# Kernel tuning notes

Hardware: AMD Instinct MI355X
Metric: run time of the kernel (lower is better)

Reference implementation:

```python
import jax, jax.numpy as jnp
import numpy as np

N_NODES = 100000
N_EDGES = 1600000
F_IN = 128
F_HID = 128
BN_EPS = 1e-5


def setup_inputs() -> dict:
    key = jax.random.key(0)
    ks = jax.random.split(key, 8)
    x = jax.random.normal(ks[0], (N_NODES, F_IN), dtype=jnp.float32)
    edge_row = jax.random.randint(ks[1], (N_EDGES,), 0, N_NODES, dtype=jnp.int32)
    edge_col = jax.random.randint(ks[2], (N_EDGES,), 0, N_NODES, dtype=jnp.int32)
    edge_weight = jax.random.uniform(ks[3], (N_EDGES,), dtype=jnp.float32)
    # Glorot-ish init for the two GCN layer weights
    W1 = jax.random.normal(ks[4], (F_IN, F_HID), dtype=jnp.float32) * (1.0 / np.sqrt(F_IN))
    b1 = jnp.zeros((F_HID,), dtype=jnp.float32)
    W2 = jax.random.normal(ks[5], (F_HID, F_HID), dtype=jnp.float32) * (1.0 / np.sqrt(F_HID))
    b2 = jnp.zeros((F_HID,), dtype=jnp.float32)
    gamma = jnp.ones((F_HID,), dtype=jnp.float32)
    beta = jnp.zeros((F_HID,), dtype=jnp.float32)
    return {"x": x, "edge_row": edge_row, "edge_col": edge_col,
            "edge_weight": edge_weight, "W1": W1, "b1": b1,
            "W2": W2, "b2": b2, "gamma": gamma, "beta": beta}


def _spmm(row, col, w, dense):
    # sparse [N,N] @ dense [N,F] via gather + segment_sum (COO)
    gathered = dense[col] * w[:, None]           # [E, F]
    return jax.ops.segment_sum(gathered, row, num_segments=N_NODES)


def _batchnorm(h, gamma, beta):
    # BatchNorm1d in training mode: batch statistics over node dim
    mean = jnp.mean(h, axis=0)
    var = jnp.var(h, axis=0)
    return gamma * (h - mean) * jax.lax.rsqrt(var + BN_EPS) + beta


def reference(x, edge_row, edge_col, edge_weight, W1, b1, W2, b2, gamma, beta):
    # Layer 1: GCN conv = adj @ (x @ W1) + b1
    h = _spmm(edge_row, edge_col, edge_weight, x @ W1) + b1
    # BN -> ReLU (dropout is identity in deterministic/eval reference)
    h = jax.nn.relu(_batchnorm(h, gamma, beta))
    # Layer 2: GCN conv
    out = _spmm(edge_row, edge_col, edge_weight, h @ W2) + b2
    return out
```

## Files before the change

kernel.cpp:

```cpp
#include <hip/hip_runtime.h>

#define F    128
#define FQ   32
#define FU   64
#define RPB  128
#define BSH  7
#define TILE 2048
#define SCAP 4096
#define LSTR 68

typedef __attribute__((ext_vector_type(8))) short short8;
typedef __attribute__((ext_vector_type(4))) float f32x4;
typedef __attribute__((ext_vector_type(4))) unsigned int u32x4;

__device__ __forceinline__ unsigned int f2bf2(float a, float b) {
    unsigned int ua = __float_as_uint(a);
    unsigned int ub = __float_as_uint(b);
    ua = (ua + 0x7fffu + ((ua >> 16) & 1u)) >> 16;
    ub = (ub + 0x7fffu + ((ub >> 16) & 1u)) >> 16;
    return ua | (ub << 16);
}
__device__ __forceinline__ unsigned short f2bf1(float a) {
    unsigned int ua = __float_as_uint(a);
    return (unsigned short)((ua + 0x7fffu + ((ua >> 16) & 1u)) >> 16);
}

__global__ __launch_bounds__(256) void wconv_kernel(const float* __restrict__ W1,
                                                    const float* __restrict__ W2,
                                                    unsigned int* __restrict__ Wt1,
                                                    unsigned int* __restrict__ Wt2) {
    const float* W = blockIdx.x ? W2 : W1;
    unsigned int* Wt = blockIdx.x ? Wt2 : Wt1;
    int f = threadIdx.x & 127;
    int kh = (threadIdx.x >> 7) * 64;
    #pragma unroll
    for (int k8 = 0; k8 < 8; ++k8) {
        int k0 = kh + k8 * 8;
        float v[8];
        #pragma unroll
        for (int i = 0; i < 8; ++i) v[i] = W[(size_t)(k0 + i) * F + f];
        uint4 pk;
        pk.x = f2bf2(v[0], v[1]);
        pk.y = f2bf2(v[2], v[3]);
        pk.z = f2bf2(v[4], v[5]);
        pk.w = f2bf2(v[6], v[7]);
        *(uint4*)&Wt[f * 64 + k0 / 2] = pk;
    }
}

template <bool BN>
__global__ __launch_bounds__(256) void gemm_kernel(const void* __restrict__ Xv,
                                                   const unsigned int* __restrict__ Wt,
                                                   const float* __restrict__ stats,
                                                   const float* __restrict__ gamma,
                                                   const float* __restrict__ beta,
                                                   float invN,
                                                   unsigned int* __restrict__ Hb,
                                                   int nNodes) {
    __shared__ unsigned int XtU[64 * LSTR];
    __shared__ unsigned int WtU[128 * LSTR];

    const int tid = threadIdx.x;
    const int bn0 = blockIdx.x * 64;

    {
        int f = tid >> 1;
        int kh = (tid & 1) * 32;
        const uint4* Wg4 = (const uint4*)Wt;
        #pragma unroll
        for (int j = 0; j < 8; ++j) {
            uint4 pk = Wg4[f * 16 + (kh >> 2) + j];
            *(uint4*)&WtU[f * LSTR + kh + j * 4] = pk;
        }
    }
    {
        const int kq = tid & 31;
        float4 a4, c4;
        if (BN) {
            float4 s  = ((const float4*)stats)[kq];
            float4 sq = ((const float4*)(stats + 128))[kq];
            float4 g4 = ((const float4*)gamma)[kq];
            float4 b4 = ((const float4*)beta)[kq];
            float m;
            m = s.x * invN; a4.x = g4.x * rsqrtf(sq.x * invN - m * m + 1e-5f); c4.x = b4.x - m * a4.x;
            m = s.y * invN; a4.y = g4.y * rsqrtf(sq.y * invN - m * m + 1e-5f); c4.y = b4.y - m * a4.y;
            m = s.z * invN; a4.z = g4.z * rsqrtf(sq.z * invN - m * m + 1e-5f); c4.z = b4.z - m * a4.z;
            m = s.w * invN; a4.w = g4.w * rsqrtf(sq.w * invN - m * m + 1e-5f); c4.w = b4.w - m * a4.w;
        }
        #pragma unroll
        for (int it = 0; it < 8; ++it) {
            int i = tid + it * 256;
            int n = i >> 5;
            int node = bn0 + n;
            uint2 pk = make_uint2(0u, 0u);
            if (BN) {
                uint2 raw = make_uint2(0u, 0u);
                if (node < nNodes) raw = ((const uint2*)Xv)[(size_t)node * 32 + kq];
                float4 v;
                v.x = __uint_as_float(raw.x << 16);
                v.y = __uint_as_float(raw.x & 0xffff0000u);
                v.z = __uint_as_float(raw.y << 16);
                v.w = __uint_as_float(raw.y & 0xffff0000u);
                v.x = fmaxf(fmaf(a4.x, v.x, c4.x), 0.f);
                v.y = fmaxf(fmaf(a4.y, v.y, c4.y), 0.f);
                v.z = fmaxf(fmaf(a4.z, v.z, c4.z), 0.f);
                v.w = fmaxf(fmaf(a4.w, v.w, c4.w), 0.f);
                pk = make_uint2(f2bf2(v.x, v.y), f2bf2(v.z, v.w));
            } else {
                float4 v = make_float4(0.f, 0.f, 0.f, 0.f);
                if (node < nNodes) v = ((const float4*)Xv)[(size_t)node * FQ + kq];
                pk = make_uint2(f2bf2(v.x, v.y), f2bf2(v.z, v.w));
            }
            *(uint2*)&XtU[n * LSTR + kq * 2] = pk;
        }
    }
    __syncthreads();

    const int l = tid & 63;
    const int wv = tid >> 6;
    const int quad = l >> 4, lo = l & 15;
    const int fb = wv * 32;

    f32x4 acc[4][2];
    #pragma unroll
    for (int nt = 0; nt < 4; ++nt)
        #pragma unroll
        for (int ft = 0; ft < 2; ++ft) acc[nt][ft] = (f32x4){0.f, 0.f, 0.f, 0.f};

    #pragma unroll
    for (int kc = 0; kc < 4; ++kc) {
        int koff = kc * 16 + quad * 4;
        short8 a[4], b[2];
        #pragma unroll
        for (int nt = 0; nt < 4; ++nt)
            a[nt] = *(const short8*)&XtU[(nt * 16 + lo) * LSTR + koff];
        #pragma unroll
        for (int ft = 0; ft < 2; ++ft)
            b[ft] = *(const short8*)&WtU[(fb + ft * 16 + lo) * LSTR + koff];
        #pragma unroll
        for (int nt = 0; nt < 4; ++nt)
            #pragma unroll
            for (int ft = 0; ft < 2; ++ft)
                acc[nt][ft] = __builtin_amdgcn_mfma_f32_16x16x32_bf16(
                    a[nt], b[ft], acc[nt][ft], 0, 0, 0);
    }

    unsigned short* Hs = (unsigned short*)Hb;
    #pragma unroll
    for (int nt = 0; nt < 4; ++nt) {
        #pragma unroll
        for (int reg = 0; reg < 4; ++reg) {
            int node = bn0 + nt * 16 + quad * 4 + reg;
            if (node < nNodes) {
                #pragma unroll
                for (int ft = 0; ft < 2; ++ft)
                    Hs[(size_t)node * F + fb + ft * 16 + lo] = f2bf1(acc[nt][ft][reg]);
            }
        }
    }
}

__global__ __launch_bounds__(256) void histo_kernel(const int* __restrict__ row,
                                                    int* __restrict__ hist,
                                                    int NB, int E) {
    __shared__ int h[1024];
    int t = threadIdx.x;
    for (int i = t; i < NB; i += 256) h[i] = 0;
    __syncthreads();
    int base = blockIdx.x * TILE + t * 8;
    if (base + 7 < E) {
        int4 a = ((const int4*)row)[(base >> 2) + 0];
        int4 b = ((const int4*)row)[(base >> 2) + 1];
        atomicAdd(&h[a.x >> BSH], 1); atomicAdd(&h[a.y >> BSH], 1);
        atomicAdd(&h[a.z >> BSH], 1); atomicAdd(&h[a.w >> BSH], 1);
        atomicAdd(&h[b.x >> BSH], 1); atomicAdd(&h[b.y >> BSH], 1);
        atomicAdd(&h[b.z >> BSH], 1); atomicAdd(&h[b.w >> BSH], 1);
    } else {
        for (int j = 0; j < 8; ++j)
            if (base + j < E) atomicAdd(&h[row[base + j] >> BSH], 1);
    }
    __syncthreads();
    for (int i = t; i < NB; i += 256) hist[(size_t)blockIdx.x * NB + i] = h[i];
}

__global__ __launch_bounds__(256) void btot_kernel(const int* __restrict__ hist,
                                                   int* __restrict__ total,
                                                   int nT, int NB) {
    int b = blockIdx.x;
    int s = 0;
    for (int t = threadIdx.x; t < nT; t += 256) s += hist[(size_t)t * NB + b];
    __shared__ int red[256];
    red[threadIdx.x] = s;
    __syncthreads();
    for (int o = 128; o > 0; o >>= 1) {
        if (threadIdx.x < o) red[threadIdx.x] += red[threadIdx.x + o];
        __syncthreads();
    }
    if (threadIdx.x == 0) total[b] = red[0];
}

__global__ __launch_bounds__(1024) void bstart_kernel(const int* __restrict__ total,
                                                      int* __restrict__ start,
                                                      int NB, int E) {
    __shared__ int sh[1024];
    int t = threadIdx.x;
    int v = (t < NB) ? total[t] : 0;
    sh[t] = v;
    __syncthreads();
    #pragma unroll
    for (int o = 1; o < 1024; o <<= 1) {
        int add = (t >= o) ? sh[t - o] : 0;
        __syncthreads();
        sh[t] += add;
        __syncthreads();
    }
    if (t < NB) start[t] = sh[t] - v;
    if (t == 0) start[NB] = E;
}

__global__ __launch_bounds__(1024) void boff_kernel(const int* __restrict__ hist,
                                                    const int* __restrict__ start,
                                                    int* __restrict__ off,
                                                    int nT, int NB) {
    __shared__ int sh[1024];
    int b = blockIdx.x, t = threadIdx.x;
    int v = (t < nT) ? hist[(size_t)t * NB + b] : 0;
    sh[t] = v;
    __syncthreads();
    #pragma unroll
    for (int o = 1; o < 1024; o <<= 1) {
        int add = (t >= o) ? sh[t - o] : 0;
        __syncthreads();
        sh[t] += add;
        __syncthreads();
    }
    if (t < nT) off[(size_t)b * nT + t] = start[b] + sh[t] - v;
}

__global__ __launch_bounds__(256) void bplace_kernel(const int* __restrict__ row,
                                                     const int* __restrict__ col,
                                                     const float* __restrict__ w,
                                                     const int* __restrict__ off,
                                                     int2* __restrict__ tmp,
                                                     int nT, int NB, int E) {
    __shared__ int h[1024];
    int t = threadIdx.x, tile = blockIdx.x;
    for (int i = t; i < NB; i += 256) h[i] = 0;
    __syncthreads();
    int base = tile * TILE + t * 8;
    int r[8], c[8];
    float ww[8];
    int nv = 0;
    if (base + 7 < E) {
        int4 ra = ((const int4*)row)[(base >> 2) + 0];
        int4 rb = ((const int4*)row)[(base >> 2) + 1];
        int4 ca = ((const int4*)col)[(base >> 2) + 0];
        int4 cb = ((const int4*)col)[(base >> 2) + 1];
        float4 wa = ((const float4*)w)[(base >> 2) + 0];
        float4 wb = ((const float4*)w)[(base >> 2) + 1];
        r[0] = ra.x; r[1] = ra.y; r[2] = ra.z; r[3] = ra.w;
        r[4] = rb.x; r[5] = rb.y; r[6] = rb.z; r[7] = rb.w;
        c[0] = ca.x; c[1] = ca.y; c[2] = ca.z; c[3] = ca.w;
        c[4] = cb.x; c[5] = cb.y; c[6] = cb.z; c[7] = cb.w;
        ww[0] = wa.x; ww[1] = wa.y; ww[2] = wa.z; ww[3] = wa.w;
        ww[4] = wb.x; ww[5] = wb.y; ww[6] = wb.z; ww[7] = wb.w;
        nv = 8;
    } else {
        for (int j = 0; j < 8; ++j)
            if (base + j < E) { r[nv] = row[base + j]; c[nv] = col[base + j];
                                ww[nv] = w[base + j]; ++nv; }
    }
    #pragma unroll 8
    for (int j = 0; j < 8; ++j) {
        if (j >= nv) break;
        int b = r[j] >> BSH;
        int rank = atomicAdd(&h[b], 1);
        int pos = off[(size_t)b * nT + tile] + rank;
        tmp[pos] = make_int2(((r[j] & (RPB - 1)) << 25) | c[j], __float_as_int(ww[j]));
    }
}

__global__ __launch_bounds__(256) void bsort_kernel(const int2* __restrict__ tmp,
                                                    const int* __restrict__ start,
                                                    int2* __restrict__ pairs,
                                                    int* __restrict__ rowptr,
                                                    int N, int NB, int E) {
    __shared__ int cntB[RPB];
    __shared__ int cntS[RPB];
    __shared__ int sc[RPB];
    __shared__ int2 outP[SCAP];
    int b = blockIdx.x, t = threadIdx.x;
    int s0 = start[b], s1 = start[b + 1];
    int len = s1 - s0;
    if (len > SCAP) len = SCAP;

    if (t < RPB) cntB[t] = 0;
    __syncthreads();

    int2 p[16];
    int np = 0;
    #pragma unroll
    for (int k = 0; k < 16; ++k) {
        int i = t + k * 256;
        if (i < len) { p[k] = tmp[s0 + i]; ++np; }
    }
    #pragma unroll
    for (int k = 0; k < 16; ++k) {
        if (k >= np) break;
        atomicAdd(&cntB[((unsigned)p[k].x) >> 25], 1);
    }
    __syncthreads();
    int val = (t < RPB) ? cntB[t] : 0;
    if (t < RPB) sc[t] = val;
    __syncthreads();
    #pragma unroll
    for (int o = 1; o < RPB; o <<= 1) {
        int add = (t < RPB && t >= o) ? sc[t - o] : 0;
        __syncthreads();
        if (t < RPB) sc[t] += add;
        __syncthreads();
    }
    if (t < RPB) { int ex = sc[t] - val; cntB[t] = ex; cntS[t] = ex; }
    __syncthreads();
    #pragma unroll
    for (int k = 0; k < 16; ++k) {
        if (k >= np) break;
        int rl = ((unsigned)p[k].x) >> 25;
        int lr = atomicAdd(&cntB[rl], 1);
        outP[lr] = make_int2(p[k].x & 0x1ffffff, p[k].y);
    }
    __syncthreads();
    for (int i = t; i < len; i += 256) pairs[s0 + i] = outP[i];
    int r0 = b * RPB;
    if (t < RPB && r0 + t < N) rowptr[r0 + t] = s0 + cntS[t];
    if (b == NB - 1 && t == 0) rowptr[N] = E;
}

template <bool BF16OUT>
__global__ __launch_bounds__(256) void spmm_csr_kernel(const int* __restrict__ rowptr,
                                                       const int2* __restrict__ pairs,
                                                       const unsigned int* __restrict__ Hb,
                                                       const float* __restrict__ bias,
                                                       void* __restrict__ outv, int N) {
    int r = blockIdx.x * 4 + (threadIdx.x >> 6);
    if (r >= N) return;
    const int l = threadIdx.x & 63;
    const int g = l >> 4, q = l & 15;
    const uint4* H4 = (const uint4*)Hb;

    float acc[8];
    #pragma unroll
    for (int j = 0; j < 8; ++j) acc[j] = 0.f;

    int i = rowptr[r], end = rowptr[r + 1];

    for (; i + 16 <= end; i += 16) {
        int2 p[4];
        uint4 gv[4];
        #pragma unroll
        for (int k = 0; k < 4; ++k) p[k] = pairs[i + 4 * k + g];
        #pragma unroll
        for (int k = 0; k < 4; ++k) gv[k] = H4[(size_t)p[k].x * 16 + q];
        #pragma unroll
        for (int k = 0; k < 4; ++k) {
            float wt = __int_as_float(p[k].y);
            unsigned int uu[4] = {gv[k].x, gv[k].y, gv[k].z, gv[k].w};
            #pragma unroll
            for (int j = 0; j < 4; ++j) {
                acc[2 * j]     = fmaf(wt, __uint_as_float(uu[j] << 16), acc[2 * j]);
                acc[2 * j + 1] = fmaf(wt, __uint_as_float(uu[j] & 0xffff0000u), acc[2 * j + 1]);
            }
        }
    }
    for (; i + 4 <= end; i += 4) {
        int2 p = pairs[i + g];
        uint4 gv = H4[(size_t)p.x * 16 + q];
        float wt = __int_as_float(p.y);
        unsigned int uu[4] = {gv.x, gv.y, gv.z, gv.w};
        #pragma unroll
        for (int j = 0; j < 4; ++j) {
            acc[2 * j]     = fmaf(wt, __uint_as_float(uu[j] << 16), acc[2 * j]);
            acc[2 * j + 1] = fmaf(wt, __uint_as_float(uu[j] & 0xffff0000u), acc[2 * j + 1]);
        }
    }
    if (i < end) {
        int e = i + g;
        int2 p = (e < end) ? pairs[e] : make_int2(0, 0);
        uint4 gv = H4[(size_t)p.x * 16 + q];
        float wt = __int_as_float(p.y);
        unsigned int uu[4] = {gv.x, gv.y, gv.z, gv.w};
        #pragma unroll
        for (int j = 0; j < 4; ++j) {
            acc[2 * j]     = fmaf(wt, __uint_as_float(uu[j] << 16), acc[2 * j]);
            acc[2 * j + 1] = fmaf(wt, __uint_as_float(uu[j] & 0xffff0000u), acc[2 * j + 1]);
        }
    }

    #pragma unroll
    for (int j = 0; j < 8; ++j) {
        acc[j] += __shfl_xor(acc[j], 16, 64);
        acc[j] += __shfl_xor(acc[j], 32, 64);
    }

    if (g == 0) {
        if (bias) {
            float4 b0 = ((const float4*)bias)[q * 2];
            float4 b1 = ((const float4*)bias)[q * 2 + 1];
            acc[0] += b0.x; acc[1] += b0.y; acc[2] += b0.z; acc[3] += b0.w;
            acc[4] += b1.x; acc[5] += b1.y; acc[6] += b1.z; acc[7] += b1.w;
        }
        if (BF16OUT) {
            uint4 pk;
            pk.x = f2bf2(acc[0], acc[1]);
            pk.y = f2bf2(acc[2], acc[3]);
            pk.z = f2bf2(acc[4], acc[5]);
            pk.w = f2bf2(acc[6], acc[7]);
            ((uint4*)outv)[(size_t)r * 16 + q] = pk;
        } else {
            f32x4 v0 = (f32x4){acc[0], acc[1], acc[2], acc[3]};
            f32x4 v1 = (f32x4){acc[4], acc[5], acc[6], acc[7]};
            f32x4* O = (f32x4*)outv;
            __builtin_nontemporal_store(v0, &O[(size_t)r * 32 + q * 2]);
            __builtin_nontemporal_store(v1, &O[(size_t)r * 32 + q * 2 + 1]);
        }
    }
}

__global__ __launch_bounds__(256) void bnstats_kernel(const unsigned int* __restrict__ Hu,
                                                      float* __restrict__ sums,
                                                      int nNodes) {
    int u = threadIdx.x & 63;
    int g = threadIdx.x >> 6;
    int stride = gridDim.x * 4;
    float s0 = 0.f, s1 = 0.f, q0 = 0.f, q1 = 0.f;
    for (int n = blockIdx.x * 4 + g; n < nNodes; n += stride) {
        unsigned int v = Hu[(size_t)n * FU + u];
        float a = __uint_as_float(v << 16);
        float b = __uint_as_float(v & 0xffff0000u);
        s0 += a; s1 += b;
        q0 = fmaf(a, a, q0); q1 = fmaf(b, b, q1);
    }
    __shared__ float4 red[256];
    red[threadIdx.x] = make_float4(s0, s1, q0, q1);
    __syncthreads();
    if (g == 0) {
        float4 r0 = red[u], r1 = red[64 + u], r2 = red[128 + u], r3 = red[192 + u];
        atomicAdd(&sums[2 * u],           r0.x + r1.x + r2.x + r3.x);
        atomicAdd(&sums[2 * u + 1],       r0.y + r1.y + r2.y + r3.y);
        atomicAdd(&sums[128 + 2 * u],     r0.z + r1.z + r2.z + r3.z);
        atomicAdd(&sums[128 + 2 * u + 1], r0.w + r1.w + r2.w + r3.w);
    }
}

extern "C" void kernel_launch(void* const* d_in, const int* in_sizes, int n_in,
                              void* d_out, int out_size, void* d_ws, size_t ws_size,
                              hipStream_t stream) {
    const float* x    = (const float*)d_in[0];
    const int*   erow = (const int*)d_in[1];
    const int*   ecol = (const int*)d_in[2];
    const float* ew   = (const float*)d_in[3];
    const float* W1   = (const float*)d_in[4];
    const float* W2   = (const float*)d_in[6];
    const float* b2   = (const float*)d_in[7];
    const float* gmm  = (const float*)d_in[8];
    const float* beta = (const float*)d_in[9];
    float* out = (float*)d_out;

    const int N = in_sizes[0] / F;
    const int E = in_sizes[1];

    const int NB = (N + RPB - 1) / RPB;
    const int nT = (E + TILE - 1) / TILE;

    unsigned int* buf1   = (unsigned int*)d_ws;
    unsigned int* Hb     = buf1 + (size_t)N * FU;
    float*        stats  = (float*)(Hb + (size_t)N * FU);
    unsigned int* wt1    = (unsigned int*)(stats + 256);
    unsigned int* wt2    = wt1 + 8192;
    int*          rowptr = (int*)(wt2 + 8192);
    int*          start  = rowptr + N + 2;
    int*          total  = start + 1028;
    int*          hist   = total + 1024;
    int*          off    = hist + (size_t)nT * NB;
    int2*         tmp    = (int2*)(off + (size_t)NB * nT);
    int2*         pairs  = tmp + E;

    const int gemmGrid = (N + 63) / 64;
    const int spmmGrid = (N + 3) / 4;

    hipMemsetAsync(stats, 0, 256 * sizeof(float), stream);

    wconv_kernel<<<2, 256, 0, stream>>>(W1, W2, wt1, wt2);

    histo_kernel<<<nT, 256, 0, stream>>>(erow, hist, NB, E);
    btot_kernel<<<NB, 256, 0, stream>>>(hist, total, nT, NB);
    bstart_kernel<<<1, 1024, 0, stream>>>(total, start, NB, E);
    boff_kernel<<<NB, 1024, 0, stream>>>(hist, start, off, nT, NB);
    bplace_kernel<<<nT, 256, 0, stream>>>(erow, ecol, ew, off, tmp, nT, NB, E);
    bsort_kernel<<<NB, 256, 0, stream>>>(tmp, start, pairs, rowptr, N, NB, E);

    gemm_kernel<false><<<gemmGrid, 256, 0, stream>>>(x, wt1, nullptr, nullptr,
                                                     nullptr, 0.f, Hb, N);
    spmm_csr_kernel<true><<<spmmGrid, 256, 0, stream>>>(rowptr, pairs, Hb,
                                                        nullptr, buf1, N);
    bnstats_kernel<<<400, 256, 0, stream>>>(buf1, stats, N);
    gemm_kernel<true><<<gemmGrid, 256, 0, stream>>>(buf1, wt2, stats, gmm, beta,
                                                    1.0f / (float)N, Hb, N);
    spmm_csr_kernel<false><<<spmmGrid, 256, 0, stream>>>(rowptr, pairs, Hb,
                                                         b2, out, N);
}
```

Measured before the change: 397.2 us.

## Merge preprocessing launches and co-schedule first GEMM with edge placement

Folds the weight conversion into the histogram kernel, merges the bucket-start scan into the per-bucket offset kernel, and runs the first-layer GEMM blocks in the same launch as the edge bucket placement. Each tile now covers 8192 edges instead of 2048, so there are fewer histogram rows and offset scan entries. The aim is to cut launch count and let the independent GEMM overlap the memory-bound placement pass. In exchange, every offset block recomputes the bucket-total scan, and fewer tiles means less parallelism in the histogram and placement phases.

```diff
diff --git a/kernel.cpp b/kernel.cpp
--- a/kernel.cpp
+++ b/kernel.cpp
@@ -5,13 +5,12 @@
 #define FU   64
 #define RPB  128
 #define BSH  7
-#define TILE 2048
+#define TILE 8192
 #define SCAP 4096
 #define LSTR 68
 
 typedef __attribute__((ext_vector_type(8))) short short8;
 typedef __attribute__((ext_vector_type(4))) float f32x4;
-typedef __attribute__((ext_vector_type(4))) unsigned int u32x4;
 
 __device__ __forceinline__ unsigned int f2bf2(float a, float b) {
     unsigned int ua = __float_as_uint(a);
@@ -25,43 +24,19 @@
     return (unsigned short)((ua + 0x7fffu + ((ua >> 16) & 1u)) >> 16);
 }
 
-__global__ __launch_bounds__(256) void wconv_kernel(const float* __restrict__ W1,
-                                                    const float* __restrict__ W2,
-                                                    unsigned int* __restrict__ Wt1,
-                                                    unsigned int* __restrict__ Wt2) {
-    const float* W = blockIdx.x ? W2 : W1;
-    unsigned int* Wt = blockIdx.x ? Wt2 : Wt1;
-    int f = threadIdx.x & 127;
-    int kh = (threadIdx.x >> 7) * 64;
-    #pragma unroll
-    for (int k8 = 0; k8 < 8; ++k8) {
-        int k0 = kh + k8 * 8;
-        float v[8];
-        #pragma unroll
-        for (int i = 0; i < 8; ++i) v[i] = W[(size_t)(k0 + i) * F + f];
-        uint4 pk;
-        pk.x = f2bf2(v[0], v[1]);
-        pk.y = f2bf2(v[2], v[3]);
-        pk.z = f2bf2(v[4], v[5]);
-        pk.w = f2bf2(v[6], v[7]);
-        *(uint4*)&Wt[f * 64 + k0 / 2] = pk;
-    }
-}
-
 template <bool BN>
-__global__ __launch_bounds__(256) void gemm_kernel(const void* __restrict__ Xv,
-                                                   const unsigned int* __restrict__ Wt,
-                                                   const float* __restrict__ stats,
-                                                   const float* __restrict__ gamma,
-                                                   const float* __restrict__ beta,
-                                                   float invN,
-                                                   unsigned int* __restrict__ Hb,
-                                                   int nNodes) {
-    __shared__ unsigned int XtU[64 * LSTR];
-    __shared__ unsigned int WtU[128 * LSTR];
-
+__device__ __forceinline__ void gemm_body(unsigned int* __restrict__ XtU,
+                                          unsigned int* __restrict__ WtU,
+                                          const void* __restrict__ Xv,
+                                          const unsigned int* __restrict__ Wt,
+                                          const float* __restrict__ stats,
+                                          const float* __restrict__ gamma,
+                                          const float* __restrict__ beta,
+                                          float invN,
+                                          unsigned int* __restrict__ Hb,
+                                          int nNodes, int bid) {
     const int tid = threadIdx.x;
-    const int bn0 = blockIdx.x * 64;
+    const int bn0 = bid * 64;
 
     {
         int f = tid >> 1;
@@ -160,27 +135,69 @@
     }
 }
 
-__global__ __launch_bounds__(256) void histo_kernel(const int* __restrict__ row,
-                                                    int* __restrict__ hist,
-                                                    int NB, int E) {
+template <bool BN>
+__global__ __launch_bounds__(256) void gemm_kernel(const void* __restrict__ Xv,
+                                                   const unsigned int* __restrict__ Wt,
+                                                   const float* __restrict__ stats,
+                                                   const float* __restrict__ gamma,
+                                                   const float* __restrict__ beta,
+                                                   float invN,
+                                                   unsigned int* __restrict__ Hb,
+                                                   int nNodes) {
+    __shared__ unsigned int shm[192 * LSTR];
+    gemm_body<BN>(shm, shm + 64 * LSTR, Xv, Wt, stats, gamma, beta, invN, Hb,
+                  nNodes, blockIdx.x);
+}
+
+__global__ __launch_bounds__(256) void wchisto_kernel(const float* __restrict__ W1,
+                                                      const float* __restrict__ W2,
+                                                      unsigned int* __restrict__ Wt1,
+                                                      unsigned int* __restrict__ Wt2,
+                                                      const int* __restrict__ row,
+                                                      int* __restrict__ hist,
+                                                      int NB, int E) {
     __shared__ int h[1024];
-    int t = threadIdx.x;
+    if (blockIdx.x < 2) {
+        const float* W = blockIdx.x ? W2 : W1;
+        unsigned int* Wt = blockIdx.x ? Wt2 : Wt1;
+        int f = threadIdx.x & 127;
+        int kh = (threadIdx.x >> 7) * 64;
+        #pragma unroll
+        for (int k8 = 0; k8 < 8; ++k8) {
+            int k0 = kh + k8 * 8;
+            float v[8];
+            #pragma unroll
+            for (int i = 0; i < 8; ++i) v[i] = W[(size_t)(k0 + i) * F + f];
+            uint4 pk;
+            pk.x = f2bf2(v[0], v[1]);
+            pk.y = f2bf2(v[2], v[3]);
+            pk.z = f2bf2(v[4], v[5]);
+            pk.w = f2bf2(v[6], v[7]);
+            *(uint4*)&Wt[f * 64 + k0 / 2] = pk;
+        }
+        return;
+    }
+    const int tile = blockIdx.x - 2;
+    const int t = threadIdx.x;
     for (int i = t; i < NB; i += 256) h[i] = 0;
     __syncthreads();
-    int base = blockIdx.x * TILE + t * 8;
-    if (base + 7 < E) {
-        int4 a = ((const int4*)row)[(base >> 2) + 0];
-        int4 b = ((const int4*)row)[(base >> 2) + 1];
-        atomicAdd(&h[a.x >> BSH], 1); atomicAdd(&h[a.y >> BSH], 1);
-        atomicAdd(&h[a.z >> BSH], 1); atomicAdd(&h[a.w >> BSH], 1);
-        atomicAdd(&h[b.x >> BSH], 1); atomicAdd(&h[b.y >> BSH], 1);
-        atomicAdd(&h[b.z >> BSH], 1); atomicAdd(&h[b.w >> BSH], 1);
-    } else {
-        for (int j = 0; j < 8; ++j)
-            if (base + j < E) atomicAdd(&h[row[base + j] >> BSH], 1);
-    }
-    __syncthreads();
-    for (int i = t; i < NB; i += 256) hist[(size_t)blockIdx.x * NB + i] = h[i];
+    #pragma unroll 1
+    for (int c = 0; c < TILE / 2048; ++c) {
+        int base = tile * TILE + c * 2048 + t * 8;
+        if (base + 7 < E) {
+            int4 a = ((const int4*)row)[(base >> 2) + 0];
+            int4 b = ((const int4*)row)[(base >> 2) + 1];
+            atomicAdd(&h[a.x >> BSH], 1); atomicAdd(&h[a.y >> BSH], 1);
+            atomicAdd(&h[a.z >> BSH], 1); atomicAdd(&h[a.w >> BSH], 1);
+            atomicAdd(&h[b.x >> BSH], 1); atomicAdd(&h[b.y >> BSH], 1);
+            atomicAdd(&h[b.z >> BSH], 1); atomicAdd(&h[b.w >> BSH], 1);
+        } else {
+            for (int j = 0; j < 8; ++j)
+                if (base + j < E) atomicAdd(&h[row[base + j] >> BSH], 1);
+        }
+    }
+    __syncthreads();
+    for (int i = t; i < NB; i += 256) hist[(size_t)tile * NB + i] = h[i];
 }
 
 __global__ __launch_bounds__(256) void btot_kernel(const int* __restrict__ hist,
@@ -199,13 +216,15 @@
     if (threadIdx.x == 0) total[b] = red[0];
 }
 
-__global__ __launch_bounds__(1024) void bstart_kernel(const int* __restrict__ total,
-                                                      int* __restrict__ start,
-                                                      int NB, int E) {
+__global__ __launch_bounds__(1024) void boffs_kernel(const int* __restrict__ hist,
+                                                     const int* __restrict__ total,
+                                                     int* __restrict__ start,
+                                                     int* __restrict__ off,
+                                                     int nT, int NB, int E) {
     __shared__ int sh[1024];
-    int t = threadIdx.x;
-    int v = (t < NB) ? total[t] : 0;
-    sh[t] = v;
+    const int b = blockIdx.x, t = threadIdx.x;
+    int tv = (t < NB) ? total[t] : 0;
+    sh[t] = tv;
     __syncthreads();
     #pragma unroll
     for (int o = 1; o < 1024; o <<= 1) {
@@ -214,16 +233,12 @@
         sh[t] += add;
         __syncthreads();
     }
-    if (t < NB) start[t] = sh[t] - v;
-    if (t == 0) start[NB] = E;
-}
-
-__global__ __launch_bounds__(1024) void boff_kernel(const int* __restrict__ hist,
-                                                    const int* __restrict__ start,
-                                                    int* __restrict__ off,
-                                                    int nT, int NB) {
-    __shared__ int sh[1024];
-    int b = blockIdx.x, t = threadIdx.x;
+    const int s0 = (b > 0) ? sh[b - 1] : 0;
+    if (t == 0) {
+        start[b] = s0;
+        if (b == NB - 1) start[NB] = E;
+    }
+    __syncthreads();
     int v = (t < nT) ? hist[(size_t)t * NB + b] : 0;
     sh[t] = v;
     __syncthreads();
@@ -234,49 +249,70 @@
         sh[t] += add;
         __syncthreads();
     }
-    if (t < nT) off[(size_t)b * nT + t] = start[b] + sh[t] - v;
-}
-
-__global__ __launch_bounds__(256) void bplace_kernel(const int* __restrict__ row,
+    if (t < nT) off[(size_t)b * nT + t] = s0 + sh[t] - v;
+}
+
+__device__ __forceinline__ void bplace_body(int* __restrict__ h,
+                                            const int* __restrict__ row,
+                                            const int* __restrict__ col,
+                                            const float* __restrict__ w,
+                                            const int* __restrict__ off,
+                                            int2* __restrict__ tmp,
+                                            int nT, int NB, int E, int tile) {
+    const int t = threadIdx.x;
+    for (int i = t; i < NB; i += 256) h[i] = 0;
+    __syncthreads();
+    #pragma unroll 1
+    for (int c = 0; c < TILE / 2048; ++c) {
+        int base = tile * TILE + c * 2048 + t * 8;
+        int r[8], cc[8];
+        float ww[8];
+        int nv = 0;
+        if (base + 7 < E) {
+            int4 ra = ((const int4*)row)[(base >> 2) + 0];
+            int4 rb = ((const int4*)row)[(base >> 2) + 1];
+            int4 ca = ((const int4*)col)[(base >> 2) + 0];
+            int4 cb = ((const int4*)col)[(base >> 2) + 1];
+            float4 wa = ((const float4*)w)[(base >> 2) + 0];
+            float4 wb = ((const float4*)w)[(base >> 2) + 1];
+            r[0] = ra.x; r[1] = ra.y; r[2] = ra.z; r[3] = ra.w;
+            r[4] = rb.x; r[5] = rb.y; r[6] = rb.z; r[7] = rb.w;
+            cc[0] = ca.x; cc[1] = ca.y; cc[2] = ca.z; cc[3] = ca.w;
+            cc[4] = cb.x; cc[5] = cb.y; cc[6] = cb.z; cc[7] = cb.w;
+            ww[0] = wa.x; ww[1] = wa.y; ww[2] = wa.z; ww[3] = wa.w;
+            ww[4] = wb.x; ww[5] = wb.y; ww[6] = wb.z; ww[7] = wb.w;
+            nv = 8;
+        } else {
+            for (int j = 0; j < 8; ++j)
+                if (base + j < E) { r[nv] = row[base + j]; cc[nv] = col[base + j];
+                                    ww[nv] = w[base + j]; ++nv; }
+        }
+        #pragma unroll 8
+        for (int j = 0; j < 8; ++j) {
+            if (j >= nv) break;
+            int b = r[j] >> BSH;
+            int rank = atomicAdd(&h[b], 1);
+            int pos = off[(size_t)b * nT + tile] + rank;
+            tmp[pos] = make_int2(((r[j] & (RPB - 1)) << 25) | cc[j], __float_as_int(ww[j]));
+        }
+    }
+}
+
+__global__ __launch_bounds__(256) void bpgemm_kernel(const int* __restrict__ row,
                                                      const int* __restrict__ col,
                                                      const float* __restrict__ w,
                                                      const int* __restrict__ off,
                                                      int2* __restrict__ tmp,
-                                                     int nT, int NB, int E) {
-    __shared__ int h[1024];
-    int t = threadIdx.x, tile = blockIdx.x;
-    for (int i = t; i < NB; i += 256) h[i] = 0;
-    __syncthreads();
-    int base = tile * TILE + t * 8;
-    int r[8], c[8];
-    float ww[8];
-    int nv = 0;
-    if (base + 7 < E) {
-        int4 ra = ((const int4*)row)[(base >> 2) + 0];
-        int4 rb = ((const int4*)row)[(base >> 2) + 1];
-        int4 ca = ((const int4*)col)[(base >> 2) + 0];
-        int4 cb = ((const int4*)col)[(base >> 2) + 1];
-        float4 wa = ((const float4*)w)[(base >> 2) + 0];
-        float4 wb = ((const float4*)w)[(base >> 2) + 1];
-        r[0] = ra.x; r[1] = ra.y; r[2] = ra.z; r[3] = ra.w;
-        r[4] = rb.x; r[5] = rb.y; r[6] = rb.z; r[7] = rb.w;
-        c[0] = ca.x; c[1] = ca.y; c[2] = ca.z; c[3] = ca.w;
-        c[4] = cb.x; c[5] = cb.y; c[6] = cb.z; c[7] = cb.w;
-        ww[0] = wa.x; ww[1] = wa.y; ww[2] = wa.z; ww[3] = wa.w;
-        ww[4] = wb.x; ww[5] = wb.y; ww[6] = wb.z; ww[7] = wb.w;
-        nv = 8;
+                                                     const float* __restrict__ x,
+                                                     const unsigned int* __restrict__ wt1,
+                                                     unsigned int* __restrict__ Hb,
+                                                     int nT, int NB, int E, int nNodes) {
+    __shared__ unsigned int shm[192 * LSTR];
+    if (blockIdx.x < (unsigned)nT) {
+        bplace_body((int*)shm, row, col, w, off, tmp, nT, NB, E, blockIdx.x);
     } else {
-        for (int j = 0; j < 8; ++j)
-            if (base + j < E) { r[nv] = row[base + j]; c[nv] = col[base + j];
-                                ww[nv] = w[base + j]; ++nv; }
-    }
-    #pragma unroll 8
-    for (int j = 0; j < 8; ++j) {
-        if (j >= nv) break;
-        int b = r[j] >> BSH;
-        int rank = atomicAdd(&h[b], 1);
-        int pos = off[(size_t)b * nT + tile] + rank;
-        tmp[pos] = make_int2(((r[j] & (RPB - 1)) << 25) | c[j], __float_as_int(ww[j]));
+        gemm_body<false>(shm, shm + 64 * LSTR, x, wt1, nullptr, nullptr, nullptr,
+                         0.f, Hb, nNodes, blockIdx.x - nT);
     }
 }
 
@@ -490,17 +526,13 @@
 
     hipMemsetAsync(stats, 0, 256 * sizeof(float), stream);
 
-    wconv_kernel<<<2, 256, 0, stream>>>(W1, W2, wt1, wt2);
-
-    histo_kernel<<<nT, 256, 0, stream>>>(erow, hist, NB, E);
+    wchisto_kernel<<<nT + 2, 256, 0, stream>>>(W1, W2, wt1, wt2, erow, hist, NB, E);
     btot_kernel<<<NB, 256, 0, stream>>>(hist, total, nT, NB);
-    bstart_kernel<<<1, 1024, 0, stream>>>(total, start, NB, E);
-    boff_kernel<<<NB, 1024, 0, stream>>>(hist, start, off, nT, NB);
-    bplace_kernel<<<nT, 256, 0, stream>>>(erow, ecol, ew, off, tmp, nT, NB, E);
+    boffs_kernel<<<NB, 1024, 0, stream>>>(hist, total, start, off, nT, NB, E);
+    bpgemm_kernel<<<nT + gemmGrid, 256, 0, stream>>>(erow, ecol, ew, off, tmp,
+                                                     x, wt1, Hb, nT, NB, E, N);
     bsort_kernel<<<NB, 256, 0, stream>>>(tmp, start, pairs, rowptr, N, NB, E);
 
-    gemm_kernel<false><<<gemmGrid, 256, 0, stream>>>(x, wt1, nullptr, nullptr,
-                                                     nullptr, 0.f, Hb, N);
     spmm_csr_kernel<true><<<spmmGrid, 256, 0, stream>>>(rowptr, pairs, Hb,
                                                         nullptr, buf1, N);
     bnstats_kernel<<<400, 256, 0, stream>>>(buf1, stats, N);
```

After: 385.4 us. 1.03x faster.
